# Performance work log

Hardware: AMD Instinct MI355X
Metric: run time of the kernel (lower is better)

The kernel has to match this reference:

```python
import jax, jax.numpy as jnp
import numpy as np

SCALE = 2
EPS = 1e-5  # BatchNorm2d default eps


def conv1x1(x, W, b):
    # x: [B,C,H,W], W: [O,C], b: [O]
    return jnp.einsum('bchw,oc->bohw', x, W) + b[None, :, None, None]


def maxpool(x, s):
    B, C, H, W = x.shape
    return x.reshape(B, C, H // s, s, W // s, s).max(axis=(3, 5))


def upsample_bilinear_ac(x, s):
    # bilinear upsample, align_corners=True
    B, C, H, W = x.shape
    Ho, Wo = H * s, W * s
    ys = jnp.arange(Ho) * ((H - 1) / (Ho - 1))
    xs = jnp.arange(Wo) * ((W - 1) / (Wo - 1))
    y0 = jnp.floor(ys).astype(jnp.int32)
    y1 = jnp.minimum(y0 + 1, H - 1)
    wy = (ys - y0).astype(x.dtype)
    x0 = jnp.floor(xs).astype(jnp.int32)
    x1 = jnp.minimum(x0 + 1, W - 1)
    wx = (xs - x0).astype(x.dtype)
    rows = x[:, :, y0, :] * (1 - wy)[None, None, :, None] + x[:, :, y1, :] * wy[None, None, :, None]
    return rows[:, :, :, x0] * (1 - wx) + rows[:, :, :, x1] * wx


def setup_inputs() -> dict:
    key = jax.random.key(0)
    ks = jax.random.split(key, 9)
    B, Cin, Cm, dk, H, W = 4, 64, 64, 64, 128, 128
    return {
        'x': jax.random.normal(ks[0], (B, Cin, H, W), jnp.float32),
        'memory': jax.random.normal(ks[1], (B, Cm, H, W), jnp.float32),
        'W_qkv': jax.random.normal(ks[2], (3 * dk, Cm), jnp.float32) * 0.05,
        'b_qkv': jax.random.normal(ks[3], (3 * dk,), jnp.float32) * 0.05,
        'W_out': jax.random.normal(ks[4], (Cin, dk), jnp.float32) * 0.05,
        'b_out': jax.random.normal(ks[5], (Cin,), jnp.float32) * 0.05,
        'bn_gamma': jax.random.uniform(ks[6], (Cin,), jnp.float32, 0.5, 1.5),
        'bn_beta': jax.random.normal(ks[7], (Cin,), jnp.float32) * 0.05,
        'gamma': jax.random.normal(ks[8], (1,), jnp.float32) * 0.1,
    }


def reference(x, memory, W_qkv, b_qkv, W_out, b_out, bn_gamma, bn_beta, gamma):
    d_k = W_qkv.shape[0] // 3
    qkv = conv1x1(memory, W_qkv, b_qkv)
    qkv = maxpool(qkv, SCALE)
    q, k, v = jnp.split(qkv, 3, axis=1)
    B, C, H, W = v.shape
    q = q.reshape(B, C, H * W).transpose(0, 2, 1)  # [B,N,C]
    k = k.reshape(B, C, H * W)                      # [B,C,N]
    v = v.reshape(B, C, H * W).transpose(0, 2, 1)   # [B,N,C]
    scale = jnp.asarray(d_k, x.dtype) ** 0.5
    attn = jax.nn.softmax(jnp.einsum('bnc,bcm->bnm', q, k) / scale, axis=-1)
    S = jnp.einsum('bnm,bmc->bnc', attn, v).transpose(0, 2, 1).reshape(B, C, H, W)
    S = upsample_bilinear_ac(S, SCALE)
    S = conv1x1(S, W_out, b_out)
    # BatchNorm2d (training mode: biased batch stats over B,H,W)
    mean = S.mean(axis=(0, 2, 3), keepdims=True)
    var = S.var(axis=(0, 2, 3), keepdims=True)
    S = (S - mean) / jnp.sqrt(var + EPS) * bn_gamma[None, :, None, None] + bn_beta[None, :, None, None]
    return x + gamma[0] * S
```

## Files before the change

### kernel.cpp

```cpp
#include <hip/hip_runtime.h>
#include <stdint.h>

typedef unsigned short u16;
typedef unsigned int   u32;
typedef __attribute__((ext_vector_type(8))) __bf16 bf16x8;
typedef __attribute__((ext_vector_type(4))) float  f32x4;
typedef __attribute__((ext_vector_type(2))) float  f32x2;
typedef __attribute__((ext_vector_type(4))) u32    u32x4;
typedef __attribute__((ext_vector_type(2))) u32    u32x2;

#define QSCALE 0.18033688011112042f

__device__ __forceinline__ u16 f2bf(float x) {
  u32 u = __builtin_bit_cast(u32, x);
  u = (u + 0x7FFFu + ((u >> 16) & 1u)) >> 16;
  return (u16)u;
}

__device__ __forceinline__ u32 cvt_pk_bf16(float lo, float hi) {
  u32 r;
  asm("v_cvt_pk_bf16_f32 %0, %1, %2" : "=v"(r) : "v"(lo), "v"(hi));
  return r;
}

__global__ __launch_bounds__(512) void k_qkvpool(
    const float* __restrict__ mem, const float* __restrict__ Wqkv,
    const float* __restrict__ bqkv, const float* __restrict__ Wout,
    u16* __restrict__ Q, u16* __restrict__ K, u16* __restrict__ V,
    float* __restrict__ stats)
{
  const int oy = blockIdx.x, b = blockIdx.y, t = threadIdx.x;
  const int w = t >> 6, l4 = t & 15, lh = (t >> 4) & 3;
  const int wq = w & 3, wp = w >> 2;

  if (oy == 0 && b == 0 && t < 128) stats[t] = 0.f;

  __shared__ __align__(16) u16 lds[49152];
  u16* mlds  = lds;
  u16* wlds  = lds + 16384;
  u16* qlds  = lds + 28672;
  u16* klds  = lds + 32768;
  u16* vldsT = lds + 36864;
  u16* wolds = lds + 40960;
  u16* vplds = lds + 45056;

  float bias[3][4];
  #pragma unroll
  for (int j = 0; j < 3; ++j)
    #pragma unroll
    for (int r = 0; r < 4; ++r) {
      int oc = wq * 48 + 16 * j + lh * 4 + r;
      float bv = bqkv[oc];
      bias[j][r] = (oc < 64) ? bv * QSCALE : bv;
    }

  {
    const float* src = mem + ((size_t)b * 64) * 16384 + 2 * oy * 128;
    #pragma unroll
    for (int i = 0; i < 8; ++i) {
      int g = t + 512 * i;
      int px = g & 255, c0 = (g >> 8) * 4;
      float f0 = src[(size_t)(c0 + 0) * 16384 + px];
      float f1 = src[(size_t)(c0 + 1) * 16384 + px];
      float f2 = src[(size_t)(c0 + 2) * 16384 + px];
      float f3 = src[(size_t)(c0 + 3) * 16384 + px];
      u32x2 pk;
      pk[0] = (u32)f2bf(f0) | ((u32)f2bf(f1) << 16);
      pk[1] = (u32)f2bf(f2) | ((u32)f2bf(f3) << 16);
      *(u32x2*)(mlds + px * 64 + (((c0 * 2) ^ ((px & 7) << 4)) >> 1)) = pk;
    }
  }
  {
    #pragma unroll
    for (int i = 0; i < 6; ++i) {
      int g = t + 512 * i;
      int oc = g >> 4, c0 = (g & 15) * 4;
      f32x4 wv = *(const f32x4*)(Wqkv + oc * 64 + c0);
      u32x2 pk;
      pk[0] = (u32)f2bf(wv[0]) | ((u32)f2bf(wv[1]) << 16);
      pk[1] = (u32)f2bf(wv[2]) | ((u32)f2bf(wv[3]) << 16);
      *(u32x2*)(wlds + oc * 64 + (((c0 * 2) ^ ((oc & 7) << 4)) >> 1)) = pk;
    }
  }
  {
    #pragma unroll
    for (int i = 0; i < 2; ++i) {
      int g = t + 512 * i;
      int oc = g >> 4, c0 = (g & 15) * 4;
      f32x4 wv = *(const f32x4*)(Wout + oc * 64 + c0);
      u32x2 pk;
      pk[0] = (u32)f2bf(wv[0]) | ((u32)f2bf(wv[1]) << 16);
      pk[1] = (u32)f2bf(wv[2]) | ((u32)f2bf(wv[3]) << 16);
      *(u32x2*)(wolds + oc * 64 + (((c0 * 2) ^ ((oc & 7) << 4)) >> 1)) = pk;
    }
  }
  __syncthreads();

  const int sw  = (l4 & 7) << 4;
  const int oF0 = ((lh * 16) ^ sw) >> 1;
  const int oF1 = ((64 + lh * 16) ^ sw) >> 1;
  bf16x8 af[3][2];
  #pragma unroll
  for (int j = 0; j < 3; ++j) {
    const u16* ar = wlds + (wq * 48 + 16 * j + l4) * 64;
    af[j][0] = *(const bf16x8*)(ar + oF0);
    af[j][1] = *(const bf16x8*)(ar + oF1);
  }

  #pragma unroll 2
  for (int tpi = 0; tpi < 4; ++tpi) {
    const int tp = wp * 4 + tpi;
    const u16* br0 = mlds + (16 * tp + l4) * 64;
    const u16* br1 = mlds + (128 + 16 * tp + l4) * 64;
    bf16x8 b00 = *(const bf16x8*)(br0 + oF0);
    bf16x8 b01 = *(const bf16x8*)(br0 + oF1);
    bf16x8 b10 = *(const bf16x8*)(br1 + oF0);
    bf16x8 b11 = *(const bf16x8*)(br1 + oF1);
    const int ox = 8 * tp + (l4 >> 1);
    #pragma unroll
    for (int j = 0; j < 3; ++j) {
      f32x4 a0 = {0, 0, 0, 0}, a1 = {0, 0, 0, 0};
      a0 = __builtin_amdgcn_mfma_f32_16x16x32_bf16(af[j][0], b00, a0, 0, 0, 0);
      a0 = __builtin_amdgcn_mfma_f32_16x16x32_bf16(af[j][1], b01, a0, 0, 0, 0);
      a1 = __builtin_amdgcn_mfma_f32_16x16x32_bf16(af[j][0], b10, a1, 0, 0, 0);
      a1 = __builtin_amdgcn_mfma_f32_16x16x32_bf16(af[j][1], b11, a1, 0, 0, 0);
      const int ocj = wq * 48 + 16 * j;
      const float sc = (ocj < 64) ? QSCALE : 1.0f;
      #pragma unroll
      for (int r = 0; r < 4; ++r) {
        float m = fmaxf(a0[r], a1[r]);
        m = fmaxf(m, __shfl_xor(m, 1, 64));
        u16 val = f2bf(m * sc + bias[j][r]);
        if ((l4 & 1) == 0) {
          int oc = ocj + lh * 4 + r;
          if (ocj < 64)       qlds[ox * 64 + oc]        = val;
          else if (ocj < 128) klds[ox * 64 + (oc - 64)] = val;
          else {
            int vch = oc - 128;
            vldsT[ox * 64 + (((vch * 2) ^ ((ox & 7) << 4)) >> 1)] = val;
          }
        }
      }
    }
  }
  __syncthreads();

  {
    const u16* ar = wolds + (wq * 16 + l4) * 64;
    bf16x8 aw0 = *(const bf16x8*)(ar + oF0);
    bf16x8 aw1 = *(const bf16x8*)(ar + oF1);
    #pragma unroll
    for (int nti = 0; nti < 2; ++nti) {
      const int nt = wp * 2 + nti;
      const u16* brow = vldsT + (nt * 16 + l4) * 64;
      bf16x8 bw0 = *(const bf16x8*)(brow + oF0);
      bf16x8 bw1 = *(const bf16x8*)(brow + oF1);
      f32x4 u = {0, 0, 0, 0};
      u = __builtin_amdgcn_mfma_f32_16x16x32_bf16(aw0, bw0, u, 0, 0, 0);
      u = __builtin_amdgcn_mfma_f32_16x16x32_bf16(aw1, bw1, u, 0, 0, 0);
      #pragma unroll
      for (int r = 0; r < 4; ++r) {
        int oc = wq * 16 + lh * 4 + r;
        vplds[oc * 64 + nt * 16 + l4] = f2bf(u[r]);
      }
    }
  }
  __syncthreads();

  {
    int r = t >> 3, e8 = (t & 7) * 8;
    size_t nb = (size_t)oy * 64;
    *(u32x4*)(Q + ((size_t)b * 4096 + nb + r) * 64 + e8) = *(const u32x4*)(qlds + r * 64 + e8);
    *(u32x4*)(K + ((size_t)b * 4096 + nb + r) * 64 + e8) = *(const u32x4*)(klds + r * 64 + e8);
    *(u32x4*)(V + ((size_t)b * 64 + r) * 4096 + nb + e8) = *(const u32x4*)(vplds + r * 64 + e8);
  }
}

__global__ __launch_bounds__(1024, 4) void k_attn(
    const u16* __restrict__ Q, const u16* __restrict__ K,
    const u16* __restrict__ V, const float* __restrict__ bo,
    float* __restrict__ Sa)
{
  const int qb = blockIdx.x, b = blockIdx.y, t = threadIdx.x;
  const int w = t >> 6, l4 = t & 15, lh = (t >> 4) & 3;
  const int sgrp = w >> 2, wq = w & 3;

  __shared__ __align__(16) u16 kvbuf[16384 + 18432];

  u16* kt_w = kvbuf + sgrp * 4096;
  u16* vt_w = kvbuf + 16384 + sgrp * 4608;

  const int qrow = qb * 64 + wq * 16 + l4;
  const u16* qp = Q + ((size_t)b * 4096 + qrow) * 64 + lh * 8;
  bf16x8 qa0 = *(const bf16x8*)qp;
  bf16x8 qa1 = *(const bf16x8*)(qp + 32);

  f32x4 ot[4] = {{0,0,0,0},{0,0,0,0},{0,0,0,0},{0,0,0,0}};
  float lr = 0.f;

  const int tl = t & 255;
  const int skr = tl >> 2, skc = tl & 3;
  const u16* kgp = K + ((size_t)b * 4096 + sgrp * 1024 + skr) * 64 + skc * 16;
  const u16* vgp = V + ((size_t)b * 64 + skr) * 4096 + sgrp * 1024 + skc * 16;
  const u32 fbw = (u32)(((skr & 3) | (((skr >> 3) & 1) << 2)) << 4);
  u16* kwp0 = kt_w + skr * 64 + ((((u32)(skc * 32))      ^ fbw) >> 1);
  u16* kwp1 = kt_w + skr * 64 + ((((u32)(skc * 32 + 16)) ^ fbw) >> 1);
  u16* vwp  = vt_w + skr * 72 + skc * 16;

  const int rbase = ((l4 >> 2) << 3) + (l4 & 3);
  const int fbr   = ((l4 & 3) | (((l4 >> 2) & 1) << 2)) << 4;
  const int offL  = ((lh * 16) ^ fbr) >> 1;
  const int offH  = offL ^ 32;

  u32x4 rk0 = *(const u32x4*)kgp;
  u32x4 rk1 = *(const u32x4*)(kgp + 8);
  u32x4 rv0 = *(const u32x4*)vgp;
  u32x4 rv1 = *(const u32x4*)(vgp + 8);

  #pragma unroll 1
  for (int kti = 0; kti < 16; ++kti) {
    *(u32x4*)kwp0 = rk0;
    *(u32x4*)kwp1 = rk1;
    *(u32x4*)vwp = rv0;
    *(u32x4*)(vwp + 8) = rv1;
    __syncthreads();

    if (kti < 15) {
      rk0 = *(const u32x4*)(kgp + (kti + 1) * 4096);
      rk1 = *(const u32x4*)(kgp + (kti + 1) * 4096 + 8);
      rv0 = *(const u32x4*)(vgp + (kti + 1) * 64);
      rv1 = *(const u32x4*)(vgp + (kti + 1) * 64 + 8);
    }

    #pragma unroll
    for (int ss = 0; ss < 2; ++ss) {
      const u16* kr0 = kt_w + (ss * 32 + rbase) * 64;
      const u16* kr1 = kr0 + 4 * 64;
      bf16x8 vf0 = *(const bf16x8*)(vt_w + (l4)      * 72 + ss * 32 + lh * 8);
      bf16x8 vf1 = *(const bf16x8*)(vt_w + (16 + l4) * 72 + ss * 32 + lh * 8);
      bf16x8 vf2 = *(const bf16x8*)(vt_w + (32 + l4) * 72 + ss * 32 + lh * 8);
      bf16x8 vf3 = *(const bf16x8*)(vt_w + (48 + l4) * 72 + ss * 32 + lh * 8);
      bf16x8 k00 = *(const bf16x8*)(kr0 + offL);
      bf16x8 k01 = *(const bf16x8*)(kr0 + offH);
      bf16x8 k10 = *(const bf16x8*)(kr1 + offL);
      bf16x8 k11 = *(const bf16x8*)(kr1 + offH);

      f32x4 s0 = {0, 0, 0, 0}, s1 = {0, 0, 0, 0};
      s0 = __builtin_amdgcn_mfma_f32_16x16x32_bf16(k00, qa0, s0, 0, 0, 0);
      s0 = __builtin_amdgcn_mfma_f32_16x16x32_bf16(k01, qa1, s0, 0, 0, 0);
      s1 = __builtin_amdgcn_mfma_f32_16x16x32_bf16(k10, qa0, s1, 0, 0, 0);
      s1 = __builtin_amdgcn_mfma_f32_16x16x32_bf16(k11, qa1, s1, 0, 0, 0);

      float p0[4], p1[4];
      #pragma unroll
      for (int r = 0; r < 4; ++r) {
        p0[r] = exp2f(s0[r]);
        p1[r] = exp2f(s1[r]);
        lr += p0[r] + p1[r];
      }
      u32x4 pw;
      pw[0] = cvt_pk_bf16(p0[0], p0[1]);
      pw[1] = cvt_pk_bf16(p0[2], p0[3]);
      pw[2] = cvt_pk_bf16(p1[0], p1[1]);
      pw[3] = cvt_pk_bf16(p1[2], p1[3]);
      bf16x8 pf = __builtin_bit_cast(bf16x8, pw);

      ot[0] = __builtin_amdgcn_mfma_f32_16x16x32_bf16(vf0, pf, ot[0], 0, 0, 0);
      ot[1] = __builtin_amdgcn_mfma_f32_16x16x32_bf16(vf1, pf, ot[1], 0, 0, 0);
      ot[2] = __builtin_amdgcn_mfma_f32_16x16x32_bf16(vf2, pf, ot[2], 0, 0, 0);
      ot[3] = __builtin_amdgcn_mfma_f32_16x16x32_bf16(vf3, pf, ot[3], 0, 0, 0);
    }
    __syncthreads();
  }

  lr += __shfl_xor(lr, 16, 64);
  lr += __shfl_xor(lr, 32, 64);

  float* opb = (float*)kvbuf;
  float* mlb = (float*)(kvbuf + 32768);
  #pragma unroll
  for (int d = 0; d < 4; ++d)
    #pragma unroll
    for (int r = 0; r < 4; ++r)
      opb[w * 1024 + (16 * d + lh * 4 + r) * 16 + l4] = ot[d][r];
  if (lh == 0) mlb[w * 16 + l4] = lr;
  __syncthreads();

  const int ch = t >> 4, q0v = (t & 15) * 4;
  const float bout_c = bo[ch];
  f32x4 res;
  #pragma unroll
  for (int j = 0; j < 4; ++j) {
    int q = q0v + j, wq2 = q >> 4, ql = q & 15;
    float L = mlb[(wq2)*16      + ql] + mlb[(4 + wq2)*16  + ql]
            + mlb[(8 + wq2)*16  + ql] + mlb[(12 + wq2)*16 + ql];
    float O = opb[(wq2)*1024      + ch * 16 + ql]
            + opb[(4 + wq2)*1024  + ch * 16 + ql]
            + opb[(8 + wq2)*1024  + ch * 16 + ql]
            + opb[(12 + wq2)*1024 + ch * 16 + ql];
    res[j] = O / L + bout_c;
  }
  *(f32x4*)(Sa + ((size_t)b * 64 + ch) * 4096 + (size_t)qb * 64 + q0v) = res;
}

__global__ __launch_bounds__(1024) void k_stats(const float* __restrict__ U,
                                                float* __restrict__ stats)
{
  const int c = blockIdx.x & 63, b = blockIdx.x >> 6, t = threadIdx.x;
  __shared__ __align__(16) float up[4096];
  __shared__ float red[32];
  *(f32x4*)&up[t * 4] = *(const f32x4*)(U + ((size_t)b * 64 + c) * 4096 + t * 4);
  __syncthreads();
  const float R = 0.49606299212598425f;
  float sum = 0.f, ssq = 0.f;
  #pragma unroll 4
  for (int i = 0; i < 16; ++i) {
    int px = t + 1024 * i;
    int yo = px >> 7, xo = px & 127;
    float ys = yo * R; int y0 = (int)ys; float wy = ys - y0; int y1 = min(y0 + 1, 63);
    float xs = xo * R; int x0 = (int)xs; float wx = xs - x0; int x1 = min(x0 + 1, 63);
    const float* r0 = up + y0 * 64; const float* r1 = up + y1 * 64;
    float v0 = r0[x0] * (1.f - wx) + r0[x1] * wx;
    float v1 = r1[x0] * (1.f - wx) + r1[x1] * wx;
    float v = v0 * (1.f - wy) + v1 * wy;
    sum += v; ssq += v * v;
  }
  #pragma unroll
  for (int d = 32; d >= 1; d >>= 1) {
    sum += __shfl_down(sum, d, 64);
    ssq += __shfl_down(ssq, d, 64);
  }
  if ((t & 63) == 0) { red[t >> 6] = sum; red[16 + (t >> 6)] = ssq; }
  __syncthreads();
  if (t == 0) {
    float s = 0.f, q = 0.f;
    #pragma unroll
    for (int i = 0; i < 16; ++i) { s += red[i]; q += red[16 + i]; }
    atomicAdd(&stats[c], s);
    atomicAdd(&stats[64 + c], q);
  }
}

__global__ __launch_bounds__(1024) void k_apply(
    const float* __restrict__ U, const float* __restrict__ stats,
    const float* __restrict__ x, const float* __restrict__ bng,
    const float* __restrict__ bnb, const float* __restrict__ gam,
    float* __restrict__ out)
{
  const int c = blockIdx.x & 63, b = blockIdx.x >> 6, t = threadIdx.x;
  __shared__ __align__(16) float up[4096];
  *(f32x4*)&up[t * 4] = *(const f32x4*)(U + ((size_t)b * 64 + c) * 4096 + t * 4);
  __syncthreads();
  const float inv = 1.0f / 65536.0f;
  float mean = stats[c] * inv;
  float var  = stats[64 + c] * inv - mean * mean;
  float rsig = rsqrtf(var + 1e-5f);
  float g = gam[0];
  float A  = g * bng[c] * rsig;
  float Bc = g * (bnb[c] - mean * rsig * bng[c]);
  const float R = 0.49606299212598425f;
  const size_t base = ((size_t)b * 64 + c) * 16384;
  #pragma unroll 4
  for (int i = 0; i < 16; ++i) {
    int px = t + 1024 * i;
    int yo = px >> 7, xo = px & 127;
    float ys = yo * R; int y0 = (int)ys; float wy = ys - y0; int y1 = min(y0 + 1, 63);
    float xs = xo * R; int x0 = (int)xs; float wx = xs - x0; int x1 = min(x0 + 1, 63);
    const float* r0 = up + y0 * 64; const float* r1 = up + y1 * 64;
    float v0 = r0[x0] * (1.f - wx) + r0[x1] * wx;
    float v1 = r1[x0] * (1.f - wx) + r1[x1] * wx;
    float v = v0 * (1.f - wy) + v1 * wy;
    out[base + px] = x[base + px] + v * A + Bc;
  }
}

extern "C" void kernel_launch(void* const* d_in, const int* in_sizes, int n_in,
                              void* d_out, int out_size, void* d_ws, size_t ws_size,
                              hipStream_t stream)
{
  const float* x      = (const float*)d_in[0];
  const float* memory = (const float*)d_in[1];
  const float* Wqkv   = (const float*)d_in[2];
  const float* bqkv   = (const float*)d_in[3];
  const float* Wout   = (const float*)d_in[4];
  const float* bout   = (const float*)d_in[5];
  const float* bng    = (const float*)d_in[6];
  const float* bnb    = (const float*)d_in[7];
  const float* gamma  = (const float*)d_in[8];

  char* ws = (char*)d_ws;
  u16*   Q     = (u16*)(ws + 0);
  u16*   Kk    = (u16*)(ws + (2u << 20));
  u16*   Vt    = (u16*)(ws + (4u << 20));
  float* U     = (float*)(ws + (10u << 20));
  float* stats = (float*)(ws + (14u << 20));
  float* out   = (float*)d_out;

  k_qkvpool<<<dim3(64, 4), 512, 0, stream>>>(memory, Wqkv, bqkv, Wout, Q, Kk, Vt, stats);
  k_attn   <<<dim3(64, 4), 1024, 0, stream>>>(Q, Kk, Vt, bout, U);
  k_stats  <<<256, 1024, 0, stream>>>(U, stats);
  k_apply  <<<256, 1024, 0, stream>>>(U, stats, x, bng, bnb, gamma, out);
}
```

Before: 61.71 us.

## Halve attention block to 512 threads, each wave handling two query tiles

The attention kernel now runs with 8 waves instead of 16, and each wave processes two 16-row query groups against the same K/V fragments read from shared memory. This reuses each LDS K/V load for twice the MFMA work and halves the per-block thread count, with each thread staging twice as much K/V per tile. The epilogue is reorganized to reduce partial sums across the four key-split waves using vectorized LDS reads. The cost is higher register pressure per thread (doubled accumulators) and fewer waves for hiding latency.

```diff
diff --git a/kernel.cpp b/kernel.cpp
--- a/kernel.cpp
+++ b/kernel.cpp
@@ -176,60 +176,85 @@
   }
 }
 
-__global__ __launch_bounds__(1024, 4) void k_attn(
+__global__ __launch_bounds__(512, 2) void k_attn(
     const u16* __restrict__ Q, const u16* __restrict__ K,
     const u16* __restrict__ V, const float* __restrict__ bo,
     float* __restrict__ Sa)
 {
   const int qb = blockIdx.x, b = blockIdx.y, t = threadIdx.x;
   const int w = t >> 6, l4 = t & 15, lh = (t >> 4) & 3;
-  const int sgrp = w >> 2, wq = w & 3;
+  const int sgrp = w & 3, qh = w >> 2;
 
   __shared__ __align__(16) u16 kvbuf[16384 + 18432];
 
   u16* kt_w = kvbuf + sgrp * 4096;
   u16* vt_w = kvbuf + 16384 + sgrp * 4608;
 
-  const int qrow = qb * 64 + wq * 16 + l4;
-  const u16* qp = Q + ((size_t)b * 4096 + qrow) * 64 + lh * 8;
-  bf16x8 qa0 = *(const bf16x8*)qp;
-  bf16x8 qa1 = *(const bf16x8*)(qp + 32);
-
-  f32x4 ot[4] = {{0,0,0,0},{0,0,0,0},{0,0,0,0},{0,0,0,0}};
-  float lr = 0.f;
-
-  const int tl = t & 255;
-  const int skr = tl >> 2, skc = tl & 3;
-  const u16* kgp = K + ((size_t)b * 4096 + sgrp * 1024 + skr) * 64 + skc * 16;
-  const u16* vgp = V + ((size_t)b * 64 + skr) * 4096 + sgrp * 1024 + skc * 16;
-  const u32 fbw = (u32)(((skr & 3) | (((skr >> 3) & 1) << 2)) << 4);
-  u16* kwp0 = kt_w + skr * 64 + ((((u32)(skc * 32))      ^ fbw) >> 1);
-  u16* kwp1 = kt_w + skr * 64 + ((((u32)(skc * 32 + 16)) ^ fbw) >> 1);
-  u16* vwp  = vt_w + skr * 72 + skc * 16;
+  bf16x8 qa[2][2];
+  #pragma unroll
+  for (int qg = 0; qg < 2; ++qg) {
+    const int qrow = qb * 64 + qh * 32 + qg * 16 + l4;
+    const u16* qp = Q + ((size_t)b * 4096 + qrow) * 64 + lh * 8;
+    qa[qg][0] = *(const bf16x8*)qp;
+    qa[qg][1] = *(const bf16x8*)(qp + 32);
+  }
+
+  f32x4 ot[2][4] = {{{0,0,0,0},{0,0,0,0},{0,0,0,0},{0,0,0,0}},
+                    {{0,0,0,0},{0,0,0,0},{0,0,0,0},{0,0,0,0}}};
+  float lr[2] = {0.f, 0.f};
+
+  const int tl = (t & 63) | (qh << 6);
+  const int skrA = tl >> 2, skcA = tl & 3;
+  const int skrB = skrA + 32;
+  const u16* kgpA = K + ((size_t)b * 4096 + sgrp * 1024 + skrA) * 64 + skcA * 16;
+  const u16* kgpB = kgpA + 32 * 64;
+  const u16* vgpA = V + ((size_t)b * 64 + skrA) * 4096 + sgrp * 1024 + skcA * 16;
+  const u16* vgpB = V + ((size_t)b * 64 + skrB) * 4096 + sgrp * 1024 + skcA * 16;
+  const u32 fbwA = (u32)(((skrA & 3) | (((skrA >> 3) & 1) << 2)) << 4);
+  const u32 fbwB = (u32)(((skrB & 3) | (((skrB >> 3) & 1) << 2)) << 4);
+  u16* kwp0A = kt_w + skrA * 64 + ((((u32)(skcA * 32))      ^ fbwA) >> 1);
+  u16* kwp1A = kt_w + skrA * 64 + ((((u32)(skcA * 32 + 16)) ^ fbwA) >> 1);
+  u16* kwp0B = kt_w + skrB * 64 + ((((u32)(skcA * 32))      ^ fbwB) >> 1);
+  u16* kwp1B = kt_w + skrB * 64 + ((((u32)(skcA * 32 + 16)) ^ fbwB) >> 1);
+  u16* vwpA  = vt_w + skrA * 72 + skcA * 16;
+  u16* vwpB  = vt_w + skrB * 72 + skcA * 16;
 
   const int rbase = ((l4 >> 2) << 3) + (l4 & 3);
   const int fbr   = ((l4 & 3) | (((l4 >> 2) & 1) << 2)) << 4;
   const int offL  = ((lh * 16) ^ fbr) >> 1;
   const int offH  = offL ^ 32;
 
-  u32x4 rk0 = *(const u32x4*)kgp;
-  u32x4 rk1 = *(const u32x4*)(kgp + 8);
-  u32x4 rv0 = *(const u32x4*)vgp;
-  u32x4 rv1 = *(const u32x4*)(vgp + 8);
+  u32x4 rk0A = *(const u32x4*)kgpA;
+  u32x4 rk1A = *(const u32x4*)(kgpA + 8);
+  u32x4 rk0B = *(const u32x4*)kgpB;
+  u32x4 rk1B = *(const u32x4*)(kgpB + 8);
+  u32x4 rv0A = *(const u32x4*)vgpA;
+  u32x4 rv1A = *(const u32x4*)(vgpA + 8);
+  u32x4 rv0B = *(const u32x4*)vgpB;
+  u32x4 rv1B = *(const u32x4*)(vgpB + 8);
 
   #pragma unroll 1
   for (int kti = 0; kti < 16; ++kti) {
-    *(u32x4*)kwp0 = rk0;
-    *(u32x4*)kwp1 = rk1;
-    *(u32x4*)vwp = rv0;
-    *(u32x4*)(vwp + 8) = rv1;
+    *(u32x4*)kwp0A = rk0A;
+    *(u32x4*)kwp1A = rk1A;
+    *(u32x4*)kwp0B = rk0B;
+    *(u32x4*)kwp1B = rk1B;
+    *(u32x4*)vwpA = rv0A;
+    *(u32x4*)(vwpA + 8) = rv1A;
+    *(u32x4*)vwpB = rv0B;
+    *(u32x4*)(vwpB + 8) = rv1B;
     __syncthreads();
 
     if (kti < 15) {
-      rk0 = *(const u32x4*)(kgp + (kti + 1) * 4096);
-      rk1 = *(const u32x4*)(kgp + (kti + 1) * 4096 + 8);
-      rv0 = *(const u32x4*)(vgp + (kti + 1) * 64);
-      rv1 = *(const u32x4*)(vgp + (kti + 1) * 64 + 8);
+      const int ko = (kti + 1) * 4096, vo = (kti + 1) * 64;
+      rk0A = *(const u32x4*)(kgpA + ko);
+      rk1A = *(const u32x4*)(kgpA + ko + 8);
+      rk0B = *(const u32x4*)(kgpB + ko);
+      rk1B = *(const u32x4*)(kgpB + ko + 8);
+      rv0A = *(const u32x4*)(vgpA + vo);
+      rv1A = *(const u32x4*)(vgpA + vo + 8);
+      rv0B = *(const u32x4*)(vgpB + vo);
+      rv1B = *(const u32x4*)(vgpB + vo + 8);
     }
 
     #pragma unroll
@@ -245,62 +270,77 @@
       bf16x8 k10 = *(const bf16x8*)(kr1 + offL);
       bf16x8 k11 = *(const bf16x8*)(kr1 + offH);
 
-      f32x4 s0 = {0, 0, 0, 0}, s1 = {0, 0, 0, 0};
-      s0 = __builtin_amdgcn_mfma_f32_16x16x32_bf16(k00, qa0, s0, 0, 0, 0);
-      s0 = __builtin_amdgcn_mfma_f32_16x16x32_bf16(k01, qa1, s0, 0, 0, 0);
-      s1 = __builtin_amdgcn_mfma_f32_16x16x32_bf16(k10, qa0, s1, 0, 0, 0);
-      s1 = __builtin_amdgcn_mfma_f32_16x16x32_bf16(k11, qa1, s1, 0, 0, 0);
-
-      float p0[4], p1[4];
       #pragma unroll
-      for (int r = 0; r < 4; ++r) {
-        p0[r] = exp2f(s0[r]);
-        p1[r] = exp2f(s1[r]);
-        lr += p0[r] + p1[r];
+      for (int qg = 0; qg < 2; ++qg) {
+        f32x4 s0 = {0, 0, 0, 0}, s1 = {0, 0, 0, 0};
+        s0 = __builtin_amdgcn_mfma_f32_16x16x32_bf16(k00, qa[qg][0], s0, 0, 0, 0);
+        s0 = __builtin_amdgcn_mfma_f32_16x16x32_bf16(k01, qa[qg][1], s0, 0, 0, 0);
+        s1 = __builtin_amdgcn_mfma_f32_16x16x32_bf16(k10, qa[qg][0], s1, 0, 0, 0);
+        s1 = __builtin_amdgcn_mfma_f32_16x16x32_bf16(k11, qa[qg][1], s1, 0, 0, 0);
+
+        float p0[4], p1[4];
+        #pragma unroll
+        for (int r = 0; r < 4; ++r) {
+          p0[r] = exp2f(s0[r]);
+          p1[r] = exp2f(s1[r]);
+          lr[qg] += p0[r] + p1[r];
+        }
+        u32x4 pw;
+        pw[0] = cvt_pk_bf16(p0[0], p0[1]);
+        pw[1] = cvt_pk_bf16(p0[2], p0[3]);
+        pw[2] = cvt_pk_bf16(p1[0], p1[1]);
+        pw[3] = cvt_pk_bf16(p1[2], p1[3]);
+        bf16x8 pf = __builtin_bit_cast(bf16x8, pw);
+
+        ot[qg][0] = __builtin_amdgcn_mfma_f32_16x16x32_bf16(vf0, pf, ot[qg][0], 0, 0, 0);
+        ot[qg][1] = __builtin_amdgcn_mfma_f32_16x16x32_bf16(vf1, pf, ot[qg][1], 0, 0, 0);
+        ot[qg][2] = __builtin_amdgcn_mfma_f32_16x16x32_bf16(vf2, pf, ot[qg][2], 0, 0, 0);
+        ot[qg][3] = __builtin_amdgcn_mfma_f32_16x16x32_bf16(vf3, pf, ot[qg][3], 0, 0, 0);
       }
-      u32x4 pw;
-      pw[0] = cvt_pk_bf16(p0[0], p0[1]);
-      pw[1] = cvt_pk_bf16(p0[2], p0[3]);
-      pw[2] = cvt_pk_bf16(p1[0], p1[1]);
-      pw[3] = cvt_pk_bf16(p1[2], p1[3]);
-      bf16x8 pf = __builtin_bit_cast(bf16x8, pw);
-
-      ot[0] = __builtin_amdgcn_mfma_f32_16x16x32_bf16(vf0, pf, ot[0], 0, 0, 0);
-      ot[1] = __builtin_amdgcn_mfma_f32_16x16x32_bf16(vf1, pf, ot[1], 0, 0, 0);
-      ot[2] = __builtin_amdgcn_mfma_f32_16x16x32_bf16(vf2, pf, ot[2], 0, 0, 0);
-      ot[3] = __builtin_amdgcn_mfma_f32_16x16x32_bf16(vf3, pf, ot[3], 0, 0, 0);
     }
     __syncthreads();
   }
 
-  lr += __shfl_xor(lr, 16, 64);
-  lr += __shfl_xor(lr, 32, 64);
+  #pragma unroll
+  for (int qg = 0; qg < 2; ++qg) {
+    lr[qg] += __shfl_xor(lr[qg], 16, 64);
+    lr[qg] += __shfl_xor(lr[qg], 32, 64);
+  }
 
   float* opb = (float*)kvbuf;
-  float* mlb = (float*)(kvbuf + 32768);
-  #pragma unroll
-  for (int d = 0; d < 4; ++d)
-    #pragma unroll
-    for (int r = 0; r < 4; ++r)
-      opb[w * 1024 + (16 * d + lh * 4 + r) * 16 + l4] = ot[d][r];
-  if (lh == 0) mlb[w * 16 + l4] = lr;
-  __syncthreads();
-
-  const int ch = t >> 4, q0v = (t & 15) * 4;
+  float* mlb = ((float*)kvbuf) + 16384;
+  #pragma unroll
+  for (int qg = 0; qg < 2; ++qg)
+    #pragma unroll
+    for (int d = 0; d < 4; ++d)
+      #pragma unroll
+      for (int r = 0; r < 4; ++r)
+        opb[w * 2048 + (16 * d + lh * 4 + r) * 32 + qg * 16 + l4] = ot[qg][d][r];
+  if (lh == 0) {
+    mlb[w * 32 + l4]      = lr[0];
+    mlb[w * 32 + 16 + l4] = lr[1];
+  }
+  __syncthreads();
+
+  const int ch = t >> 3, qq = t & 7;
   const float bout_c = bo[ch];
-  f32x4 res;
-  #pragma unroll
-  for (int j = 0; j < 4; ++j) {
-    int q = q0v + j, wq2 = q >> 4, ql = q & 15;
-    float L = mlb[(wq2)*16      + ql] + mlb[(4 + wq2)*16  + ql]
-            + mlb[(8 + wq2)*16  + ql] + mlb[(12 + wq2)*16 + ql];
-    float O = opb[(wq2)*1024      + ch * 16 + ql]
-            + opb[(4 + wq2)*1024  + ch * 16 + ql]
-            + opb[(8 + wq2)*1024  + ch * 16 + ql]
-            + opb[(12 + wq2)*1024 + ch * 16 + ql];
-    res[j] = O / L + bout_c;
-  }
-  *(f32x4*)(Sa + ((size_t)b * 64 + ch) * 4096 + (size_t)qb * 64 + q0v) = res;
+  #pragma unroll
+  for (int h = 0; h < 2; ++h) {
+    const int q0 = qq * 4;
+    f32x4 O0 = *(const f32x4*)&opb[(h * 4 + 0) * 2048 + ch * 32 + q0];
+    f32x4 O1 = *(const f32x4*)&opb[(h * 4 + 1) * 2048 + ch * 32 + q0];
+    f32x4 O2 = *(const f32x4*)&opb[(h * 4 + 2) * 2048 + ch * 32 + q0];
+    f32x4 O3 = *(const f32x4*)&opb[(h * 4 + 3) * 2048 + ch * 32 + q0];
+    f32x4 L0 = *(const f32x4*)&mlb[(h * 4 + 0) * 32 + q0];
+    f32x4 L1 = *(const f32x4*)&mlb[(h * 4 + 1) * 32 + q0];
+    f32x4 L2 = *(const f32x4*)&mlb[(h * 4 + 2) * 32 + q0];
+    f32x4 L3 = *(const f32x4*)&mlb[(h * 4 + 3) * 32 + q0];
+    f32x4 res;
+    #pragma unroll
+    for (int j = 0; j < 4; ++j)
+      res[j] = (O0[j] + O1[j] + O2[j] + O3[j]) / (L0[j] + L1[j] + L2[j] + L3[j]) + bout_c;
+    *(f32x4*)(Sa + ((size_t)b * 64 + ch) * 4096 + (size_t)qb * 64 + h * 32 + q0) = res;
+  }
 }
 
 __global__ __launch_bounds__(1024) void k_stats(const float* __restrict__ U,
@@ -397,7 +437,7 @@
   float* out   = (float*)d_out;
 
   k_qkvpool<<<dim3(64, 4), 512, 0, stream>>>(memory, Wqkv, bqkv, Wout, Q, Kk, Vt, stats);
-  k_attn   <<<dim3(64, 4), 1024, 0, stream>>>(Q, Kk, Vt, bout, U);
+  k_attn   <<<dim3(64, 4), 512, 0, stream>>>(Q, Kk, Vt, bout, U);
   k_stats  <<<256, 1024, 0, stream>>>(U, stats);
   k_apply  <<<256, 1024, 0, stream>>>(U, stats, x, bng, bnb, gamma, out);
 }
```

New measurement: 65.39 us. 1.06x slower.

## Split attention waves by key half so each wave reuses K/V fragments across two query groups

Applied to the files above, without the earlier changes.

Each wave now handles two 16-row query groups and one 32-key half of each tile instead of one query group and both halves. The K and V fragments loaded from shared memory are reused for both query groups, halving LDS reads per MFMA. The final reduction now sums eight partial results per query instead of four, using a larger shared buffer (about 130KB). That larger buffer may lower occupancy and the launch-bounds hint, and each wave also holds more accumulator registers.

```diff
diff --git a/kernel.cpp b/kernel.cpp
--- a/kernel.cpp
+++ b/kernel.cpp
@@ -183,20 +183,27 @@
 {
   const int qb = blockIdx.x, b = blockIdx.y, t = threadIdx.x;
   const int w = t >> 6, l4 = t & 15, lh = (t >> 4) & 3;
-  const int sgrp = w >> 2, wq = w & 3;
-
-  __shared__ __align__(16) u16 kvbuf[16384 + 18432];
+  const int sgrp = w >> 2;
+  const int qh = (w >> 1) & 1;
+  const int ssw = w & 1;
+
+  __shared__ __align__(16) u16 kvbuf[66560];
 
   u16* kt_w = kvbuf + sgrp * 4096;
   u16* vt_w = kvbuf + 16384 + sgrp * 4608;
 
-  const int qrow = qb * 64 + wq * 16 + l4;
-  const u16* qp = Q + ((size_t)b * 4096 + qrow) * 64 + lh * 8;
-  bf16x8 qa0 = *(const bf16x8*)qp;
-  bf16x8 qa1 = *(const bf16x8*)(qp + 32);
-
-  f32x4 ot[4] = {{0,0,0,0},{0,0,0,0},{0,0,0,0},{0,0,0,0}};
-  float lr = 0.f;
+  bf16x8 qa[2][2];
+  #pragma unroll
+  for (int qg = 0; qg < 2; ++qg) {
+    const int qrow = qb * 64 + qh * 32 + qg * 16 + l4;
+    const u16* qp = Q + ((size_t)b * 4096 + qrow) * 64 + lh * 8;
+    qa[qg][0] = *(const bf16x8*)qp;
+    qa[qg][1] = *(const bf16x8*)(qp + 32);
+  }
+
+  f32x4 ot[2][4] = {{{0,0,0,0},{0,0,0,0},{0,0,0,0},{0,0,0,0}},
+                    {{0,0,0,0},{0,0,0,0},{0,0,0,0},{0,0,0,0}}};
+  float lr[2] = {0.f, 0.f};
 
   const int tl = t & 255;
   const int skr = tl >> 2, skc = tl & 3;
@@ -232,75 +239,88 @@
       rv1 = *(const u32x4*)(vgp + (kti + 1) * 64 + 8);
     }
 
-    #pragma unroll
-    for (int ss = 0; ss < 2; ++ss) {
-      const u16* kr0 = kt_w + (ss * 32 + rbase) * 64;
+    {
+      const u16* kr0 = kt_w + (ssw * 32 + rbase) * 64;
       const u16* kr1 = kr0 + 4 * 64;
-      bf16x8 vf0 = *(const bf16x8*)(vt_w + (l4)      * 72 + ss * 32 + lh * 8);
-      bf16x8 vf1 = *(const bf16x8*)(vt_w + (16 + l4) * 72 + ss * 32 + lh * 8);
-      bf16x8 vf2 = *(const bf16x8*)(vt_w + (32 + l4) * 72 + ss * 32 + lh * 8);
-      bf16x8 vf3 = *(const bf16x8*)(vt_w + (48 + l4) * 72 + ss * 32 + lh * 8);
+      bf16x8 vf0 = *(const bf16x8*)(vt_w + (l4)      * 72 + ssw * 32 + lh * 8);
+      bf16x8 vf1 = *(const bf16x8*)(vt_w + (16 + l4) * 72 + ssw * 32 + lh * 8);
+      bf16x8 vf2 = *(const bf16x8*)(vt_w + (32 + l4) * 72 + ssw * 32 + lh * 8);
+      bf16x8 vf3 = *(const bf16x8*)(vt_w + (48 + l4) * 72 + ssw * 32 + lh * 8);
       bf16x8 k00 = *(const bf16x8*)(kr0 + offL);
       bf16x8 k01 = *(const bf16x8*)(kr0 + offH);
       bf16x8 k10 = *(const bf16x8*)(kr1 + offL);
       bf16x8 k11 = *(const bf16x8*)(kr1 + offH);
 
-      f32x4 s0 = {0, 0, 0, 0}, s1 = {0, 0, 0, 0};
-      s0 = __builtin_amdgcn_mfma_f32_16x16x32_bf16(k00, qa0, s0, 0, 0, 0);
-      s0 = __builtin_amdgcn_mfma_f32_16x16x32_bf16(k01, qa1, s0, 0, 0, 0);
-      s1 = __builtin_amdgcn_mfma_f32_16x16x32_bf16(k10, qa0, s1, 0, 0, 0);
-      s1 = __builtin_amdgcn_mfma_f32_16x16x32_bf16(k11, qa1, s1, 0, 0, 0);
-
-      float p0[4], p1[4];
       #pragma unroll
-      for (int r = 0; r < 4; ++r) {
-        p0[r] = exp2f(s0[r]);
-        p1[r] = exp2f(s1[r]);
-        lr += p0[r] + p1[r];
+      for (int qg = 0; qg < 2; ++qg) {
+        f32x4 s0 = {0, 0, 0, 0}, s1 = {0, 0, 0, 0};
+        s0 = __builtin_amdgcn_mfma_f32_16x16x32_bf16(k00, qa[qg][0], s0, 0, 0, 0);
+        s0 = __builtin_amdgcn_mfma_f32_16x16x32_bf16(k01, qa[qg][1], s0, 0, 0, 0);
+        s1 = __builtin_amdgcn_mfma_f32_16x16x32_bf16(k10, qa[qg][0], s1, 0, 0, 0);
+        s1 = __builtin_amdgcn_mfma_f32_16x16x32_bf16(k11, qa[qg][1], s1, 0, 0, 0);
+
+        float p0[4], p1[4];
+        #pragma unroll
+        for (int r = 0; r < 4; ++r) {
+          p0[r] = exp2f(s0[r]);
+          p1[r] = exp2f(s1[r]);
+          lr[qg] += p0[r] + p1[r];
+        }
+        u32x4 pw;
+        pw[0] = cvt_pk_bf16(p0[0], p0[1]);
+        pw[1] = cvt_pk_bf16(p0[2], p0[3]);
+        pw[2] = cvt_pk_bf16(p1[0], p1[1]);
+        pw[3] = cvt_pk_bf16(p1[2], p1[3]);
+        bf16x8 pf = __builtin_bit_cast(bf16x8, pw);
+
+        ot[qg][0] = __builtin_amdgcn_mfma_f32_16x16x32_bf16(vf0, pf, ot[qg][0], 0, 0, 0);
+        ot[qg][1] = __builtin_amdgcn_mfma_f32_16x16x32_bf16(vf1, pf, ot[qg][1], 0, 0, 0);
+        ot[qg][2] = __builtin_amdgcn_mfma_f32_16x16x32_bf16(vf2, pf, ot[qg][2], 0, 0, 0);
+        ot[qg][3] = __builtin_amdgcn_mfma_f32_16x16x32_bf16(vf3, pf, ot[qg][3], 0, 0, 0);
       }
-      u32x4 pw;
-      pw[0] = cvt_pk_bf16(p0[0], p0[1]);
-      pw[1] = cvt_pk_bf16(p0[2], p0[3]);
-      pw[2] = cvt_pk_bf16(p1[0], p1[1]);
-      pw[3] = cvt_pk_bf16(p1[2], p1[3]);
-      bf16x8 pf = __builtin_bit_cast(bf16x8, pw);
-
-      ot[0] = __builtin_amdgcn_mfma_f32_16x16x32_bf16(vf0, pf, ot[0], 0, 0, 0);
-      ot[1] = __builtin_amdgcn_mfma_f32_16x16x32_bf16(vf1, pf, ot[1], 0, 0, 0);
-      ot[2] = __builtin_amdgcn_mfma_f32_16x16x32_bf16(vf2, pf, ot[2], 0, 0, 0);
-      ot[3] = __builtin_amdgcn_mfma_f32_16x16x32_bf16(vf3, pf, ot[3], 0, 0, 0);
     }
     __syncthreads();
   }
 
-  lr += __shfl_xor(lr, 16, 64);
-  lr += __shfl_xor(lr, 32, 64);
+  #pragma unroll
+  for (int qg = 0; qg < 2; ++qg) {
+    lr[qg] += __shfl_xor(lr[qg], 16, 64);
+    lr[qg] += __shfl_xor(lr[qg], 32, 64);
+  }
 
   float* opb = (float*)kvbuf;
-  float* mlb = (float*)(kvbuf + 32768);
-  #pragma unroll
-  for (int d = 0; d < 4; ++d)
-    #pragma unroll
-    for (int r = 0; r < 4; ++r)
-      opb[w * 1024 + (16 * d + lh * 4 + r) * 16 + l4] = ot[d][r];
-  if (lh == 0) mlb[w * 16 + l4] = lr;
-  __syncthreads();
-
-  const int ch = t >> 4, q0v = (t & 15) * 4;
+  float* mlb = ((float*)kvbuf) + 32768;
+  #pragma unroll
+  for (int qg = 0; qg < 2; ++qg)
+    #pragma unroll
+    for (int d = 0; d < 4; ++d)
+      #pragma unroll
+      for (int r = 0; r < 4; ++r)
+        opb[w * 2048 + (16 * d + lh * 4 + r) * 32 + qg * 16 + l4] = ot[qg][d][r];
+  if (lh == 0) {
+    mlb[w * 32 + l4]      = lr[0];
+    mlb[w * 32 + 16 + l4] = lr[1];
+  }
+  __syncthreads();
+
+  const int ch = t >> 4, q0 = (t & 15) * 4;
+  const int mqh = q0 >> 5, ql = q0 & 31;
   const float bout_c = bo[ch];
+  f32x4 Osum = {0, 0, 0, 0}, Lsum = {0, 0, 0, 0};
+  #pragma unroll
+  for (int s = 0; s < 4; ++s)
+    #pragma unroll
+    for (int e = 0; e < 2; ++e) {
+      const int pw_ = 4 * s + 2 * mqh + e;
+      f32x4 Ov = *(const f32x4*)&opb[pw_ * 2048 + ch * 32 + ql];
+      f32x4 Lv = *(const f32x4*)&mlb[pw_ * 32 + ql];
+      #pragma unroll
+      for (int j = 0; j < 4; ++j) { Osum[j] += Ov[j]; Lsum[j] += Lv[j]; }
+    }
   f32x4 res;
   #pragma unroll
-  for (int j = 0; j < 4; ++j) {
-    int q = q0v + j, wq2 = q >> 4, ql = q & 15;
-    float L = mlb[(wq2)*16      + ql] + mlb[(4 + wq2)*16  + ql]
-            + mlb[(8 + wq2)*16  + ql] + mlb[(12 + wq2)*16 + ql];
-    float O = opb[(wq2)*1024      + ch * 16 + ql]
-            + opb[(4 + wq2)*1024  + ch * 16 + ql]
-            + opb[(8 + wq2)*1024  + ch * 16 + ql]
-            + opb[(12 + wq2)*1024 + ch * 16 + ql];
-    res[j] = O / L + bout_c;
-  }
-  *(f32x4*)(Sa + ((size_t)b * 64 + ch) * 4096 + (size_t)qb * 64 + q0v) = res;
+  for (int j = 0; j < 4; ++j) res[j] = Osum[j] / Lsum[j] + bout_c;
+  *(f32x4*)(Sa + ((size_t)b * 64 + ch) * 4096 + (size_t)qb * 64 + q0) = res;
 }
 
 __global__ __launch_bounds__(1024) void k_stats(const float* __restrict__ U,
```

Result: slower. 71.87 us (+16.5%).

## Double-buffer K/V register prefetch and remap attention blocks per XCD

Applied to the files above, without the earlier changes.

The attention kernel now prefetches K/V tiles two iterations ahead in two register sets, unrolling the tile loop by two so global loads have more time to land before their LDS store. It also switches to a 1-D grid and derives batch and query block from the block id, so that blocks on the same XCD (bid&7) share one batch's K/V in L2. The cost is extra registers per thread at 1024 threads per block, which could pressure occupancy.

```diff
diff --git a/kernel.cpp b/kernel.cpp
--- a/kernel.cpp
+++ b/kernel.cpp
@@ -181,7 +181,10 @@
     const u16* __restrict__ V, const float* __restrict__ bo,
     float* __restrict__ Sa)
 {
-  const int qb = blockIdx.x, b = blockIdx.y, t = threadIdx.x;
+  const int bid = blockIdx.x, t = threadIdx.x;
+  const int xcd = bid & 7;
+  const int b   = xcd >> 1;
+  const int qb  = ((bid >> 3) << 1) | (xcd & 1);
   const int w = t >> 6, l4 = t & 15, lh = (t >> 4) & 3;
   const int sgrp = w >> 2, wq = w & 3;
 
@@ -212,66 +215,83 @@
   const int offL  = ((lh * 16) ^ fbr) >> 1;
   const int offH  = offL ^ 32;
 
-  u32x4 rk0 = *(const u32x4*)kgp;
-  u32x4 rk1 = *(const u32x4*)(kgp + 8);
-  u32x4 rv0 = *(const u32x4*)vgp;
-  u32x4 rv1 = *(const u32x4*)(vgp + 8);
+  u32x4 xk0 = *(const u32x4*)kgp;
+  u32x4 xk1 = *(const u32x4*)(kgp + 8);
+  u32x4 xv0 = *(const u32x4*)vgp;
+  u32x4 xv1 = *(const u32x4*)(vgp + 8);
+  u32x4 yk0 = *(const u32x4*)(kgp + 4096);
+  u32x4 yk1 = *(const u32x4*)(kgp + 4096 + 8);
+  u32x4 yv0 = *(const u32x4*)(vgp + 64);
+  u32x4 yv1 = *(const u32x4*)(vgp + 64 + 8);
+
+#define ATTN_COMPUTE                                                          \
+    _Pragma("unroll")                                                         \
+    for (int ss = 0; ss < 2; ++ss) {                                          \
+      const u16* kr0 = kt_w + (ss * 32 + rbase) * 64;                         \
+      const u16* kr1 = kr0 + 4 * 64;                                          \
+      bf16x8 vf0 = *(const bf16x8*)(vt_w + (l4)      * 72 + ss * 32 + lh * 8);\
+      bf16x8 vf1 = *(const bf16x8*)(vt_w + (16 + l4) * 72 + ss * 32 + lh * 8);\
+      bf16x8 vf2 = *(const bf16x8*)(vt_w + (32 + l4) * 72 + ss * 32 + lh * 8);\
+      bf16x8 vf3 = *(const bf16x8*)(vt_w + (48 + l4) * 72 + ss * 32 + lh * 8);\
+      bf16x8 k00 = *(const bf16x8*)(kr0 + offL);                              \
+      bf16x8 k01 = *(const bf16x8*)(kr0 + offH);                              \
+      bf16x8 k10 = *(const bf16x8*)(kr1 + offL);                              \
+      bf16x8 k11 = *(const bf16x8*)(kr1 + offH);                              \
+      f32x4 s0 = {0, 0, 0, 0}, s1 = {0, 0, 0, 0};                             \
+      s0 = __builtin_amdgcn_mfma_f32_16x16x32_bf16(k00, qa0, s0, 0, 0, 0);    \
+      s0 = __builtin_amdgcn_mfma_f32_16x16x32_bf16(k01, qa1, s0, 0, 0, 0);    \
+      s1 = __builtin_amdgcn_mfma_f32_16x16x32_bf16(k10, qa0, s1, 0, 0, 0);    \
+      s1 = __builtin_amdgcn_mfma_f32_16x16x32_bf16(k11, qa1, s1, 0, 0, 0);    \
+      float p0[4], p1[4];                                                     \
+      _Pragma("unroll")                                                       \
+      for (int r = 0; r < 4; ++r) {                                           \
+        p0[r] = exp2f(s0[r]);                                                 \
+        p1[r] = exp2f(s1[r]);                                                 \
+        lr += p0[r] + p1[r];                                                  \
+      }                                                                       \
+      u32x4 pw;                                                               \
+      pw[0] = cvt_pk_bf16(p0[0], p0[1]);                                      \
+      pw[1] = cvt_pk_bf16(p0[2], p0[3]);                                      \
+      pw[2] = cvt_pk_bf16(p1[0], p1[1]);                                      \
+      pw[3] = cvt_pk_bf16(p1[2], p1[3]);                                      \
+      bf16x8 pf = __builtin_bit_cast(bf16x8, pw);                             \
+      ot[0] = __builtin_amdgcn_mfma_f32_16x16x32_bf16(vf0, pf, ot[0], 0, 0, 0);\
+      ot[1] = __builtin_amdgcn_mfma_f32_16x16x32_bf16(vf1, pf, ot[1], 0, 0, 0);\
+      ot[2] = __builtin_amdgcn_mfma_f32_16x16x32_bf16(vf2, pf, ot[2], 0, 0, 0);\
+      ot[3] = __builtin_amdgcn_mfma_f32_16x16x32_bf16(vf3, pf, ot[3], 0, 0, 0);\
+    }
 
   #pragma unroll 1
-  for (int kti = 0; kti < 16; ++kti) {
-    *(u32x4*)kwp0 = rk0;
-    *(u32x4*)kwp1 = rk1;
-    *(u32x4*)vwp = rv0;
-    *(u32x4*)(vwp + 8) = rv1;
+  for (int kt2 = 0; kt2 < 8; ++kt2) {
+    const int kti = kt2 * 2;
+    *(u32x4*)kwp0 = xk0;
+    *(u32x4*)kwp1 = xk1;
+    *(u32x4*)vwp = xv0;
+    *(u32x4*)(vwp + 8) = xv1;
     __syncthreads();
-
-    if (kti < 15) {
-      rk0 = *(const u32x4*)(kgp + (kti + 1) * 4096);
-      rk1 = *(const u32x4*)(kgp + (kti + 1) * 4096 + 8);
-      rv0 = *(const u32x4*)(vgp + (kti + 1) * 64);
-      rv1 = *(const u32x4*)(vgp + (kti + 1) * 64 + 8);
-    }
-
-    #pragma unroll
-    for (int ss = 0; ss < 2; ++ss) {
-      const u16* kr0 = kt_w + (ss * 32 + rbase) * 64;
-      const u16* kr1 = kr0 + 4 * 64;
-      bf16x8 vf0 = *(const bf16x8*)(vt_w + (l4)      * 72 + ss * 32 + lh * 8);
-      bf16x8 vf1 = *(const bf16x8*)(vt_w + (16 + l4) * 72 + ss * 32 + lh * 8);
-      bf16x8 vf2 = *(const bf16x8*)(vt_w + (32 + l4) * 72 + ss * 32 + lh * 8);
-      bf16x8 vf3 = *(const bf16x8*)(vt_w + (48 + l4) * 72 + ss * 32 + lh * 8);
-      bf16x8 k00 = *(const bf16x8*)(kr0 + offL);
-      bf16x8 k01 = *(const bf16x8*)(kr0 + offH);
-      bf16x8 k10 = *(const bf16x8*)(kr1 + offL);
-      bf16x8 k11 = *(const bf16x8*)(kr1 + offH);
-
-      f32x4 s0 = {0, 0, 0, 0}, s1 = {0, 0, 0, 0};
-      s0 = __builtin_amdgcn_mfma_f32_16x16x32_bf16(k00, qa0, s0, 0, 0, 0);
-      s0 = __builtin_amdgcn_mfma_f32_16x16x32_bf16(k01, qa1, s0, 0, 0, 0);
-      s1 = __builtin_amdgcn_mfma_f32_16x16x32_bf16(k10, qa0, s1, 0, 0, 0);
-      s1 = __builtin_amdgcn_mfma_f32_16x16x32_bf16(k11, qa1, s1, 0, 0, 0);
-
-      float p0[4], p1[4];
-      #pragma unroll
-      for (int r = 0; r < 4; ++r) {
-        p0[r] = exp2f(s0[r]);
-        p1[r] = exp2f(s1[r]);
-        lr += p0[r] + p1[r];
-      }
-      u32x4 pw;
-      pw[0] = cvt_pk_bf16(p0[0], p0[1]);
-      pw[1] = cvt_pk_bf16(p0[2], p0[3]);
-      pw[2] = cvt_pk_bf16(p1[0], p1[1]);
-      pw[3] = cvt_pk_bf16(p1[2], p1[3]);
-      bf16x8 pf = __builtin_bit_cast(bf16x8, pw);
-
-      ot[0] = __builtin_amdgcn_mfma_f32_16x16x32_bf16(vf0, pf, ot[0], 0, 0, 0);
-      ot[1] = __builtin_amdgcn_mfma_f32_16x16x32_bf16(vf1, pf, ot[1], 0, 0, 0);
-      ot[2] = __builtin_amdgcn_mfma_f32_16x16x32_bf16(vf2, pf, ot[2], 0, 0, 0);
-      ot[3] = __builtin_amdgcn_mfma_f32_16x16x32_bf16(vf3, pf, ot[3], 0, 0, 0);
-    }
+    if (kti + 2 < 16) {
+      xk0 = *(const u32x4*)(kgp + (kti + 2) * 4096);
+      xk1 = *(const u32x4*)(kgp + (kti + 2) * 4096 + 8);
+      xv0 = *(const u32x4*)(vgp + (kti + 2) * 64);
+      xv1 = *(const u32x4*)(vgp + (kti + 2) * 64 + 8);
+    }
+    ATTN_COMPUTE
     __syncthreads();
-  }
+    *(u32x4*)kwp0 = yk0;
+    *(u32x4*)kwp1 = yk1;
+    *(u32x4*)vwp = yv0;
+    *(u32x4*)(vwp + 8) = yv1;
+    __syncthreads();
+    if (kti + 3 < 16) {
+      yk0 = *(const u32x4*)(kgp + (kti + 3) * 4096);
+      yk1 = *(const u32x4*)(kgp + (kti + 3) * 4096 + 8);
+      yv0 = *(const u32x4*)(vgp + (kti + 3) * 64);
+      yv1 = *(const u32x4*)(vgp + (kti + 3) * 64 + 8);
+    }
+    ATTN_COMPUTE
+    __syncthreads();
+  }
+#undef ATTN_COMPUTE
 
   lr += __shfl_xor(lr, 16, 64);
   lr += __shfl_xor(lr, 32, 64);
@@ -397,7 +417,7 @@
   float* out   = (float*)d_out;
 
   k_qkvpool<<<dim3(64, 4), 512, 0, stream>>>(memory, Wqkv, bqkv, Wout, Q, Kk, Vt, stats);
-  k_attn   <<<dim3(64, 4), 1024, 0, stream>>>(Q, Kk, Vt, bout, U);
+  k_attn   <<<256, 1024, 0, stream>>>(Q, Kk, Vt, bout, U);
   k_stats  <<<256, 1024, 0, stream>>>(U, stats);
   k_apply  <<<256, 1024, 0, stream>>>(U, stats, x, bng, bnb, gamma, out);
 }
```

New measurement: 62.64 us. Within noise of the previous version (+1.5%).
